# Performance work log

Measured on AMD Instinct MI355X. Metric: run time of the kernel, lower is better.

The kernel has to match this reference:

```python
import math
import jax, jax.numpy as jnp
import numpy as np

B, N, D = 4, 4096, 1024
H, DH = 16, 64  # D == H * DH


def setup_inputs() -> dict:
    key = jax.random.key(0)
    ks = jax.random.split(key, 7)
    s = 1.0 / math.sqrt(D)
    return {
        "tens": jax.random.normal(ks[0], (B, N, D), dtype=jnp.float32),
        "Wq": jax.random.normal(ks[1], (D, D), dtype=jnp.float32) * s,
        "bq": jax.random.normal(ks[2], (D,), dtype=jnp.float32) * 0.01,
        "Wk": jax.random.normal(ks[3], (D, D), dtype=jnp.float32) * s,
        "bk": jax.random.normal(ks[4], (D,), dtype=jnp.float32) * 0.01,
        "Wv": jax.random.normal(ks[5], (D, D), dtype=jnp.float32) * s,
        "bv": jax.random.normal(ks[6], (D,), dtype=jnp.float32) * 0.01,
    }


def reference(tens, Wq, bq, Wk, bk, Wv, bv):
    b, n, d = tens.shape
    # projections (torch Linear: x @ W^T + b)
    q = (tens @ Wq.T + bq).reshape(b, n, H, DH)  # [B,N,H,DH]
    k = (tens @ Wk.T + bk).reshape(b, n, H, DH)
    v = (tens @ Wv.T + bv).reshape(b, n, H, DH)
    scale = (1.0 / math.sqrt(DH)) / math.sqrt(n)
    # No softmax between QK^T and V => linear, reassociate as Q @ (K^T V)
    # to avoid the O(N^2) attention matrix; identical math.
    ktv = jnp.einsum("bnhd,bnhe->bhde", k, v)          # [B,H,DH,DH]
    out = jnp.einsum("bnhd,bhde->bnhe", q, ktv) * scale  # [B,N,H,DH]
    return out.reshape(b, n, d)
```

## Files before the change

kernel.cpp:

```cpp
#include <hip/hip_runtime.h>

typedef unsigned short ushort_t;
typedef __attribute__((ext_vector_type(8))) __bf16 bf16x8;
typedef __attribute__((ext_vector_type(8))) unsigned short ushort8;
typedef __attribute__((ext_vector_type(4))) unsigned short ushort4_t;
typedef __attribute__((ext_vector_type(4))) float floatx4;

__device__ inline unsigned short f2bf(float f) {
  union { float f; unsigned u; } x; x.f = f;
  return (unsigned short)((x.u + 0x7FFFu + ((x.u >> 16) & 1u)) >> 16);
}
__device__ inline float bf2f(unsigned short v) {
  union { unsigned u; float f; } x; x.u = (unsigned)v << 16;
  return x.f;
}

__device__ inline void bar() {
  asm volatile("" ::: "memory");
  __builtin_amdgcn_s_barrier();
  asm volatile("" ::: "memory");
}
#define WAITV0 asm volatile("s_waitcnt vmcnt(0)" ::: "memory")

__global__ void cvt_tr(const float* __restrict__ tens, ushort_t* __restrict__ Xbf,
                       ushort_t* __restrict__ XT, float* __restrict__ spart,
                       const float* __restrict__ Wk, ushort_t* __restrict__ Wkbf,
                       const float* __restrict__ Wv, ushort_t* __restrict__ Wvbf) {
  int t = threadIdx.x;
  if (blockIdx.z == 4) {
    int flat = blockIdx.x + 16 * blockIdx.y;
    const float* in; ushort_t* out;
    if (flat < 512) { in = Wk; out = Wkbf; } else { in = Wv; out = Wvbf; flat -= 512; }
    int i = (flat * 256 + t) * 8;
    const float4* p = (const float4*)(in + i);
    float4 x = p[0], y = p[1];
    ushort8 o;
    o[0] = f2bf(x.x); o[1] = f2bf(x.y); o[2] = f2bf(x.z); o[3] = f2bf(x.w);
    o[4] = f2bf(y.x); o[5] = f2bf(y.y); o[6] = f2bf(y.z); o[7] = f2bf(y.w);
    *(ushort8*)(out + i) = o;
    return;
  }
  int b = blockIdx.z;
  int d0 = blockIdx.x * 64;
  int n0 = blockIdx.y * 64;
  __shared__ ushort_t sT[64 * 72];
  int nl = t >> 2, c16 = (t & 3) * 16;
  const float* src = tens + ((long)b << 22) + (long)(n0 + nl) * 1024 + d0 + c16;
  ushort8 o0, o1;
#pragma unroll
  for (int j = 0; j < 2; ++j) {
    float4 v0 = *(const float4*)(src + j * 8);
    float4 v1 = *(const float4*)(src + j * 8 + 4);
    ushort8 o;
    o[0] = f2bf(v0.x); o[1] = f2bf(v0.y); o[2] = f2bf(v0.z); o[3] = f2bf(v0.w);
    o[4] = f2bf(v1.x); o[5] = f2bf(v1.y); o[6] = f2bf(v1.z); o[7] = f2bf(v1.w);
#pragma unroll
    for (int i = 0; i < 8; ++i) sT[(c16 + j * 8 + i) * 72 + nl] = o[i];
    if (j == 0) o0 = o; else o1 = o;
  }
  ushort_t* xdst = Xbf + ((long)b << 22) + (long)(n0 + nl) * 1024 + d0 + c16;
  *(ushort8*)xdst = o0;
  *(ushort8*)(xdst + 8) = o1;
  __syncthreads();
  int dl = t >> 2, n16 = (t & 3) * 16;
  ushort8 t0 = *(const ushort8*)(sT + dl * 72 + n16);
  ushort8 t1 = *(const ushort8*)(sT + dl * 72 + n16 + 8);
  ushort_t* dst = XT + ((long)b << 22) + (long)(d0 + dl) * 4096 + n0 + n16;
  *(ushort8*)dst = t0;
  *(ushort8*)(dst + 8) = t1;
  float ps = 0.f;
#pragma unroll
  for (int i = 0; i < 8; ++i) ps += bf2f(t0[i]) + bf2f(t1[i]);
  ps += __shfl_xor(ps, 1);
  ps += __shfl_xor(ps, 2);
  if ((t & 3) == 0) spart[(((long)b << 6) + blockIdx.y) * 1024 + d0 + dl] = ps;
}

__device__ inline void gload_lds16(const void* g, void* l) {
  __builtin_amdgcn_global_load_lds(
      (const __attribute__((address_space(1))) unsigned int*)g,
      (__attribute__((address_space(3))) unsigned int*)l, 16, 0, 0);
}

template <int K>
__global__ __launch_bounds__(512, 2) void gemm256(
    const ushort_t* __restrict__ A, const ushort_t* __restrict__ Bm,
    const float* __restrict__ bias, float* __restrict__ C,
    int N, long sA_, long sB_, long sBias_, long sC_) {
  const int NT = K / 64;
  int gx = gridDim.x, gxy = gridDim.x * gridDim.y;
  int flat = blockIdx.x + gx * blockIdx.y + gxy * blockIdx.z;
  int total = gxy * gridDim.z;
  int per = total >> 3;
  int nf = (flat & 7) * per + (flat >> 3);
  int bz = nf / gxy; int rem = nf - bz * gxy;
  int by = rem / gx; int bx = rem - by * gx;

  A += (long)bz * sA_; Bm += (long)bz * sB_; C += (long)bz * sC_;
  bias += (long)bz * sBias_;

  __shared__ ushort_t sA[2][16384];
  __shared__ ushort_t sB[2][16384];

  int t = threadIdx.x;
  int w = t >> 6, l = t & 63;
  int wy = w >> 2, wx = w & 3;
  int quad = l >> 4, m16 = l & 15;
  int mBase = by * 256, nBase = bx * 256;

  int rp = w * 8 + (l >> 3);
  int p8 = l & 7;
  int ce = ((p8 ^ (rp & 7)) << 3);
  const ushort_t* gAp[4]; const ushort_t* gBp[4];
#pragma unroll
  for (int h = 0; h < 2; ++h)
#pragma unroll
    for (int g = 0; g < 2; ++g) {
      gAp[h * 2 + g] = A + (long)(mBase + h * 128 + g * 64 + rp) * K + ce;
      gBp[h * 2 + g] = Bm + (long)(nBase + h * 128 + g * 64 + rp) * K + ce;
    }

  int swz3 = m16 & 7;
  int aBase = wy * 8192 + m16 * 64;
  int bBase = (wx >> 1) * 8192 + ((wx & 1) * 64 + m16) * 64;

  floatx4 acc[8][4] = {};

  auto STAGE = [&](int kt, int buf) {
    int ko = kt * 64;
#pragma unroll
    for (int g = 0; g < 2; ++g) {
      gload_lds16(gAp[g] + ko,     sA[buf] + g * 4096 + w * 512);
      gload_lds16(gAp[2 + g] + ko, sA[buf] + 8192 + g * 4096 + w * 512);
      gload_lds16(gBp[g] + ko,     sB[buf] + g * 4096 + w * 512);
      gload_lds16(gBp[2 + g] + ko, sB[buf] + 8192 + g * 4096 + w * 512);
    }
  };

  STAGE(0, 0);
  WAITV0;
  bar();
  for (int kt = 0; kt < NT; ++kt) {
    int buf = kt & 1;
    if (kt + 1 < NT) STAGE(kt + 1, buf ^ 1);
    __builtin_amdgcn_sched_barrier(0);
    const ushort_t* pa = sA[buf];
    const ushort_t* pb = sB[buf];
    __builtin_amdgcn_s_setprio(1);
#pragma unroll
    for (int ks = 0; ks < 2; ++ks) {
      int ct = (((ks * 4 + quad) ^ swz3) << 3);
      bf16x8 bfr[4];
#pragma unroll
      for (int ni = 0; ni < 4; ++ni)
        bfr[ni] = *(const bf16x8*)(pb + bBase + ni * 16 * 64 + ct);
#pragma unroll
      for (int mg = 0; mg < 2; ++mg) {
        bf16x8 af[4];
#pragma unroll
        for (int i = 0; i < 4; ++i)
          af[i] = *(const bf16x8*)(pa + aBase + (mg * 4 + i) * 16 * 64 + ct);
#pragma unroll
        for (int i = 0; i < 4; ++i)
#pragma unroll
          for (int ni = 0; ni < 4; ++ni)
            acc[mg * 4 + i][ni] = __builtin_amdgcn_mfma_f32_16x16x32_bf16(
                af[i], bfr[ni], acc[mg * 4 + i][ni], 0, 0, 0);
      }
    }
    __builtin_amdgcn_s_setprio(0);
    if (kt + 1 < NT) { WAITV0; }
    bar();
  }

#pragma unroll
  for (int ni = 0; ni < 4; ++ni) {
    int n = nBase + wx * 64 + ni * 16 + m16;
    float bb = bias[n];
#pragma unroll
    for (int mi = 0; mi < 8; ++mi) {
      int m0 = mBase + wy * 128 + mi * 16 + quad * 4;
      floatx4 v = acc[mi][ni];
#pragma unroll
      for (int rr = 0; rr < 4; ++rr)
        C[(long)(m0 + rr) * N + n] = v[rr] + bb;
    }
  }
}

template <int K, bool SYM, bool UW>
__global__ void gemm64(const ushort_t* __restrict__ A, const ushort_t* __restrict__ Bm,
                       ushort_t* __restrict__ C, int N, long sA_, long sB_, long sC_,
                       const ushort_t* __restrict__ Wkbf, const ushort_t* __restrict__ Wvbf,
                       const float* __restrict__ spart, float* __restrict__ u,
                       float* __restrict__ wv_s) {
  __shared__ ushort_t sA[2][2][64 * 32];
  __shared__ ushort_t sB[2][2][64 * 32];
  int t = threadIdx.x;

  int bz, byy, bxx;
  if (SYM) {
    int flat = blockIdx.x + gridDim.x * blockIdx.y;
    int per = (gridDim.x * gridDim.y) >> 3;
    int nf = (flat & 7) * per + (flat >> 3);
    if (UW) {
      if (nf >= 544) {
        int id = nf - 544;
        int b = id & 3, which = (id >> 2) & 1, chunk = id >> 3;
        const ushort_t* W = which ? Wvbf : Wkbf;
        float* o = which ? wv_s : u;
        float* ss = (float*)sA;
        float4 a4 = {0.f, 0.f, 0.f, 0.f};
        const float* sp = spart + ((long)b << 16) + t * 4;
        for (int n0 = 0; n0 < 64; ++n0) {
          float4 v = *(const float4*)(sp + n0 * 1024);
          a4.x += v.x; a4.y += v.y; a4.z += v.z; a4.w += v.w;
        }
        *(float4*)(ss + t * 4) = a4;
        __syncthreads();
        int rr = chunk * 256 + t;
        const ushort_t* row = W + (long)rr * 1024;
        float acc = 0.f;
        for (int k = 0; k < 1024; k += 8) {
          ushort8 v = *(const ushort8*)(row + k);
#pragma unroll
          for (int i = 0; i < 8; ++i) acc += bf2f(v[i]) * ss[k + i];
        }
        o[b * 1024 + rr] = acc;
        return;
      }
    }
    bz = nf / 136;
    int tri = nf - bz * 136;
    byy = (int)((__fsqrt_rn(8.0f * tri + 1.0f) - 1.0f) * 0.5f);
    while ((byy + 1) * (byy + 2) / 2 <= tri) ++byy;
    while (byy * (byy + 1) / 2 > tri) --byy;
    bxx = tri - byy * (byy + 1) / 2;
  } else {
    int gx = gridDim.x, gxy = gridDim.x * gridDim.y;
    int flat = blockIdx.x + gx * blockIdx.y + gxy * blockIdx.z;
    int total = gxy * gridDim.z;
    int per = total >> 3;
    int nf = (flat & 7) * per + (flat >> 3);
    bz = nf / gxy; int rem = nf - bz * gxy;
    byy = rem / gx; bxx = rem - byy * gx;
  }

  A += (long)bz * sA_; Bm += (long)bz * sB_; C += (long)bz * sC_;

  int w = t >> 6, l = t & 63;
  int wy = w >> 1, wx = w & 1;
  int quad = l >> 4, m16 = l & 15;
  int mBase = byy * 64, nBase = bxx * 64;

  int r = l >> 2, pk = l & 3;
  int sCol = (pk ^ ((r >> 1) & 3)) * 8;
  int sRow = w * 16 + r;
  const ushort_t* gA = A + (long)(mBase + sRow) * K + sCol;
  const ushort_t* gB = Bm + (long)(nBase + sRow) * K + sCol;
  int lOff = w * 512;

  int swzR = (m16 >> 1) & 3;
  int aOff = (wy * 32 + m16) * 32 + (quad ^ swzR) * 8;
  int bOff = (wx * 32 + m16) * 32 + (quad ^ swzR) * 8;

  floatx4 acc[2][2] = {};
  const int NS = K / 64;

#pragma unroll
  for (int kk = 0; kk < 2; ++kk) {
    gload_lds16(gA + kk * 32, sA[0][kk] + lOff);
    gload_lds16(gB + kk * 32, sB[0][kk] + lOff);
  }
  __syncthreads();

  for (int kt = 0; kt < NS; ++kt) {
    if (kt + 1 < NS) {
      int nb = (kt + 1) & 1, ko = (kt + 1) * 64;
#pragma unroll
      for (int kk = 0; kk < 2; ++kk) {
        gload_lds16(gA + ko + kk * 32, sA[nb][kk] + lOff);
        gload_lds16(gB + ko + kk * 32, sB[nb][kk] + lOff);
      }
    }
    __builtin_amdgcn_sched_barrier(0);
    int cb = kt & 1;
#pragma unroll
    for (int kk = 0; kk < 2; ++kk) {
      bf16x8 af0 = *(const bf16x8*)(sA[cb][kk] + aOff);
      bf16x8 af1 = *(const bf16x8*)(sA[cb][kk] + aOff + 16 * 32);
      bf16x8 bf0 = *(const bf16x8*)(sB[cb][kk] + bOff);
      bf16x8 bf1 = *(const bf16x8*)(sB[cb][kk] + bOff + 16 * 32);
      acc[0][0] = __builtin_amdgcn_mfma_f32_16x16x32_bf16(af0, bf0, acc[0][0], 0, 0, 0);
      acc[0][1] = __builtin_amdgcn_mfma_f32_16x16x32_bf16(af0, bf1, acc[0][1], 0, 0, 0);
      acc[1][0] = __builtin_amdgcn_mfma_f32_16x16x32_bf16(af1, bf0, acc[1][0], 0, 0, 0);
      acc[1][1] = __builtin_amdgcn_mfma_f32_16x16x32_bf16(af1, bf1, acc[1][1], 0, 0, 0);
    }
    if (kt + 1 < NS) __syncthreads();
  }

#pragma unroll
  for (int ni = 0; ni < 2; ++ni) {
    int n = nBase + wx * 32 + ni * 16 + m16;
#pragma unroll
    for (int mi = 0; mi < 2; ++mi) {
      int m0 = mBase + wy * 32 + mi * 16 + quad * 4;
      floatx4 v = acc[mi][ni];
#pragma unroll
      for (int rr = 0; rr < 4; ++rr)
        C[(long)(m0 + rr) * N + n] = f2bf(v[rr]);
      if (SYM) {
        if (byy != bxx) {
          ushort4_t pkv;
#pragma unroll
          for (int rr = 0; rr < 4; ++rr) pkv[rr] = f2bf(v[rr]);
          *(ushort4_t*)(C + (long)n * N + m0) = pkv;
        }
      }
    }
  }
}

__global__ void ktv_part_k(const ushort_t* __restrict__ T1, const ushort_t* __restrict__ Wvbf,
                           const float* __restrict__ u, const float* __restrict__ wv_s,
                           const float* __restrict__ bk, const float* __restrict__ bv,
                           float* __restrict__ ktvp) {
  int id = blockIdx.x;
  int bh = id & 63, sl = id >> 6;
  int b = bh >> 4, h = bh & 15;
  int t = threadIdx.x, w = t >> 6, l = t & 63;
  int quad = l >> 4, m16 = l & 15;
  const ushort_t* Arow = T1 + ((long)b << 20) + (long)(h * 64 + w * 16 + m16) * 1024
                         + sl * 256 + quad * 8;
  const ushort_t* Brow = Wvbf + (long)(h * 64 + m16) * 1024 + sl * 256 + quad * 8;
  floatx4 acc[4] = {};
  for (int kt = 0; kt < 256; kt += 32) {
    bf16x8 af = *(const bf16x8*)(Arow + kt);
#pragma unroll
    for (int j = 0; j < 4; ++j) {
      bf16x8 bfv = *(const bf16x8*)(Brow + (long)j * 16 * 1024 + kt);
      acc[j] = __builtin_amdgcn_mfma_f32_16x16x32_bf16(af, bfv, acc[j], 0, 0, 0);
    }
  }
  float* p = ktvp + ((long)(sl * 64 + bh)) * 4096;
#pragma unroll
  for (int j = 0; j < 4; ++j) {
    int e = j * 16 + m16;
    float bve = bv[h * 64 + e];
    float wse = wv_s[b * 1024 + h * 64 + e] + 4096.f * bve;
#pragma unroll
    for (int rr = 0; rr < 4; ++rr) {
      int d = w * 16 + quad * 4 + rr;
      float corr = (sl == 0)
          ? (u[b * 1024 + h * 64 + d] * bve + bk[h * 64 + d] * wse) : 0.f;
      p[d * 64 + e] = acc[j][rr] + corr;
    }
  }
}

__global__ void make_w2(const float* __restrict__ Wq, const float* __restrict__ bq,
                        const float* __restrict__ ktvp, ushort_t* __restrict__ W2T,
                        float* __restrict__ bias2, float scale) {
  int bh = blockIdx.x, cq = blockIdx.y;
  int b = bh >> 4, h = bh & 15;
  __shared__ float sKTV[64 * 64];
  __shared__ float sW[64 * 64];
  int t = threadIdx.x;
  const float* kp = ktvp + (long)bh * 4096;
  for (int i = t * 4; i < 4096; i += 1024) {
    float4 v0 = *(const float4*)(kp + i);
    float4 v1 = *(const float4*)(kp + 262144 + i);
    float4 v2 = *(const float4*)(kp + 524288 + i);
    float4 v3 = *(const float4*)(kp + 786432 + i);
    float4 s;
    s.x = v0.x + v1.x + v2.x + v3.x;
    s.y = v0.y + v1.y + v2.y + v3.y;
    s.z = v0.z + v1.z + v2.z + v3.z;
    s.w = v0.w + v1.w + v2.w + v3.w;
    *(float4*)(sKTV + i) = s;
  }
  __syncthreads();
  if (cq == 0 && t < 64) {
    float s = 0.f;
    for (int d = 0; d < 64; ++d) s += bq[h * 64 + d] * sKTV[d * 64 + t];
    bias2[b * 1024 + h * 64 + t] = s * scale;
  }
  int e = t >> 2, c0 = (t & 3) * 16;
  for (int ct = cq * 256; ct < cq * 256 + 256; ct += 64) {
    __syncthreads();
    {
      int d = t >> 2, cc = (t & 3) * 16;
#pragma unroll
      for (int j = 0; j < 16; j += 4)
        *(float4*)(sW + d * 64 + cc + j) =
            *(const float4*)(Wq + (long)(h * 64 + d) * 1024 + ct + cc + j);
    }
    __syncthreads();
    float outv[16] = {};
    for (int d = 0; d < 64; ++d) {
      float kv = sKTV[d * 64 + e];
#pragma unroll
      for (int j = 0; j < 16; ++j) outv[j] += sW[d * 64 + c0 + j] * kv;
    }
    ushort8 o0, o1;
#pragma unroll
    for (int j = 0; j < 8; ++j) { o0[j] = f2bf(outv[j] * scale); o1[j] = f2bf(outv[8 + j] * scale); }
    ushort_t* dst = W2T + ((long)(b * 1024 + h * 64 + e)) * 1024 + ct + c0;
    *(ushort8*)dst = o0;
    *(ushort8*)(dst + 8) = o1;
  }
}

extern "C" void kernel_launch(void* const* d_in, const int* in_sizes, int n_in,
                              void* d_out, int out_size, void* d_ws, size_t ws_size,
                              hipStream_t stream) {
  (void)in_sizes; (void)n_in; (void)out_size; (void)ws_size;
  const float* tens = (const float*)d_in[0];
  const float* Wq = (const float*)d_in[1];
  const float* bq = (const float*)d_in[2];
  const float* Wk = (const float*)d_in[3];
  const float* bk = (const float*)d_in[4];
  const float* Wv = (const float*)d_in[5];
  const float* bv = (const float*)d_in[6];
  float* out = (float*)d_out;

  char* w = (char*)d_ws;
  ushort_t* Xbf  = (ushort_t*)(w);
  ushort_t* XT   = (ushort_t*)(w + 33554432);
  ushort_t* Wkbf = (ushort_t*)(w + 67108864);
  ushort_t* Wvbf = (ushort_t*)(w + 69206016);
  ushort_t* Gbf  = (ushort_t*)(w + 71303168);
  ushort_t* T1   = (ushort_t*)(w + 79691776);
  float*    spart= (float*)(w + 88080384);
  float*    u    = (float*)(w + 89128960);
  float*    wv_s = (float*)(w + 89145344);
  float*    ktvp = (float*)(w + 89161728);
  ushort_t* W2T  = (ushort_t*)(w + 93356032);
  float*    bias2= (float*)(w + 101744640);

  const float scale = (1.0f / 8.0f) / 64.0f;

  hipLaunchKernelGGL(cvt_tr, dim3(16, 64, 5), dim3(256), 0, stream,
                     tens, Xbf, XT, spart, Wk, Wkbf, Wv, Wvbf);

  hipLaunchKernelGGL((gemm64<4096, true, true>), dim3(144, 4, 1), dim3(256), 0, stream,
                     XT, XT, Gbf, 1024, 4194304L, 4194304L, 1048576L,
                     Wkbf, Wvbf, spart, u, wv_s);

  hipLaunchKernelGGL((gemm64<1024, false, false>), dim3(16, 16, 4), dim3(256), 0, stream,
                     Wkbf, Gbf, T1, 1024, 0L, 1048576L, 1048576L,
                     (const ushort_t*)nullptr, (const ushort_t*)nullptr,
                     (const float*)nullptr, (float*)nullptr, (float*)nullptr);

  hipLaunchKernelGGL(ktv_part_k, dim3(256), dim3(256), 0, stream,
                     T1, Wvbf, u, wv_s, bk, bv, ktvp);

  hipLaunchKernelGGL(make_w2, dim3(64, 4), dim3(256), 0, stream,
                     Wq, bq, ktvp, W2T, bias2, scale);

  hipLaunchKernelGGL((gemm256<1024>), dim3(4, 16, 4), dim3(512), 0, stream,
                     Xbf, W2T, bias2, out, 1024,
                     4194304L, 1048576L, 1024L, 4194304L);
}
```

Before: 275.1 us.

## Fuse Wk·G projection into per-head KTV kernel and vectorize final GEMM stores

The separate T1 = Wk·G GEMM and the ktv_part kernel are merged into one kernel. Each block computes its 64x256 slice of T1 for one head and batch, keeps it in shared memory as bf16, and multiplies it against Wv directly. This removes the T1 round trip through global memory and one launch. In exchange, the fused kernel has only 256 blocks with a long K=1024 loop that reads directly from global memory without LDS tiling. Separately, the final GEMM swaps its MFMA operand order so each lane holds consecutive columns, which allows float4 bias loads and float4 output stores instead of strided scalar stores.

```diff
diff --git a/kernel.cpp b/kernel.cpp
--- a/kernel.cpp
+++ b/kernel.cpp
@@ -165,7 +165,7 @@
 #pragma unroll
           for (int ni = 0; ni < 4; ++ni)
             acc[mg * 4 + i][ni] = __builtin_amdgcn_mfma_f32_16x16x32_bf16(
-                af[i], bfr[ni], acc[mg * 4 + i][ni], 0, 0, 0);
+                bfr[ni], af[i], acc[mg * 4 + i][ni], 0, 0, 0);
       }
     }
     __builtin_amdgcn_s_setprio(0);
@@ -174,16 +174,17 @@
   }
 
 #pragma unroll
-  for (int ni = 0; ni < 4; ++ni) {
-    int n = nBase + wx * 64 + ni * 16 + m16;
-    float bb = bias[n];
-#pragma unroll
-    for (int mi = 0; mi < 8; ++mi) {
-      int m0 = mBase + wy * 128 + mi * 16 + quad * 4;
+  for (int mi = 0; mi < 8; ++mi) {
+    int m = mBase + wy * 128 + mi * 16 + m16;
+    float* crow = C + (long)m * N;
+#pragma unroll
+    for (int ni = 0; ni < 4; ++ni) {
+      int n0 = nBase + wx * 64 + ni * 16 + quad * 4;
+      float4 bb = *(const float4*)(bias + n0);
       floatx4 v = acc[mi][ni];
-#pragma unroll
-      for (int rr = 0; rr < 4; ++rr)
-        C[(long)(m0 + rr) * N + n] = v[rr] + bb;
+      float4 o;
+      o.x = v[0] + bb.x; o.y = v[1] + bb.y; o.z = v[2] + bb.z; o.w = v[3] + bb.w;
+      *(float4*)(crow + n0) = o;
     }
   }
 }
@@ -321,28 +322,46 @@
   }
 }
 
-__global__ void ktv_part_k(const ushort_t* __restrict__ T1, const ushort_t* __restrict__ Wvbf,
-                           const float* __restrict__ u, const float* __restrict__ wv_s,
-                           const float* __restrict__ bk, const float* __restrict__ bv,
-                           float* __restrict__ ktvp) {
-  int id = blockIdx.x;
-  int bh = id & 63, sl = id >> 6;
+__global__ void t1ktv(const ushort_t* __restrict__ Wkbf, const ushort_t* __restrict__ Gbf,
+                      const ushort_t* __restrict__ Wvbf,
+                      const float* __restrict__ u, const float* __restrict__ wv_s,
+                      const float* __restrict__ bk, const float* __restrict__ bv,
+                      float* __restrict__ ktvp) {
+  int bh = blockIdx.x, cq = blockIdx.y;
   int b = bh >> 4, h = bh & 15;
+  __shared__ ushort_t sT1[64 * 264];
   int t = threadIdx.x, w = t >> 6, l = t & 63;
   int quad = l >> 4, m16 = l & 15;
-  const ushort_t* Arow = T1 + ((long)b << 20) + (long)(h * 64 + w * 16 + m16) * 1024
-                         + sl * 256 + quad * 8;
-  const ushort_t* Brow = Wvbf + (long)(h * 64 + m16) * 1024 + sl * 256 + quad * 8;
-  floatx4 acc[4] = {};
+
+  const ushort_t* Arow = Wkbf + (long)(h * 64 + w * 16 + m16) * 1024 + quad * 8;
+  const ushort_t* Brow = Gbf + ((long)b << 20) + (long)(cq * 256 + m16) * 1024 + quad * 8;
+  floatx4 acc1[16] = {};
+  for (int kt = 0; kt < 1024; kt += 32) {
+    bf16x8 af = *(const bf16x8*)(Arow + kt);
+#pragma unroll
+    for (int j = 0; j < 16; ++j) {
+      bf16x8 bfv = *(const bf16x8*)(Brow + (long)j * 16 * 1024 + kt);
+      acc1[j] = __builtin_amdgcn_mfma_f32_16x16x32_bf16(af, bfv, acc1[j], 0, 0, 0);
+    }
+  }
+#pragma unroll
+  for (int j = 0; j < 16; ++j)
+#pragma unroll
+    for (int rr = 0; rr < 4; ++rr)
+      sT1[(w * 16 + quad * 4 + rr) * 264 + j * 16 + m16] = f2bf(acc1[j][rr]);
+  __syncthreads();
+
+  const ushort_t* Brow2 = Wvbf + (long)(h * 64 + m16) * 1024 + cq * 256 + quad * 8;
+  floatx4 acc2[4] = {};
   for (int kt = 0; kt < 256; kt += 32) {
-    bf16x8 af = *(const bf16x8*)(Arow + kt);
+    bf16x8 af2 = *(const bf16x8*)(sT1 + (w * 16 + m16) * 264 + quad * 8 + kt);
 #pragma unroll
     for (int j = 0; j < 4; ++j) {
-      bf16x8 bfv = *(const bf16x8*)(Brow + (long)j * 16 * 1024 + kt);
-      acc[j] = __builtin_amdgcn_mfma_f32_16x16x32_bf16(af, bfv, acc[j], 0, 0, 0);
-    }
-  }
-  float* p = ktvp + ((long)(sl * 64 + bh)) * 4096;
+      bf16x8 bfv = *(const bf16x8*)(Brow2 + (long)j * 16 * 1024 + kt);
+      acc2[j] = __builtin_amdgcn_mfma_f32_16x16x32_bf16(af2, bfv, acc2[j], 0, 0, 0);
+    }
+  }
+  float* p = ktvp + ((long)(cq * 64 + bh)) * 4096;
 #pragma unroll
   for (int j = 0; j < 4; ++j) {
     int e = j * 16 + m16;
@@ -351,9 +370,9 @@
 #pragma unroll
     for (int rr = 0; rr < 4; ++rr) {
       int d = w * 16 + quad * 4 + rr;
-      float corr = (sl == 0)
+      float corr = (cq == 0)
           ? (u[b * 1024 + h * 64 + d] * bve + bk[h * 64 + d] * wse) : 0.f;
-      p[d * 64 + e] = acc[j][rr] + corr;
+      p[d * 64 + e] = acc2[j][rr] + corr;
     }
   }
 }
@@ -430,13 +449,12 @@
   ushort_t* Wkbf = (ushort_t*)(w + 67108864);
   ushort_t* Wvbf = (ushort_t*)(w + 69206016);
   ushort_t* Gbf  = (ushort_t*)(w + 71303168);
-  ushort_t* T1   = (ushort_t*)(w + 79691776);
-  float*    spart= (float*)(w + 88080384);
-  float*    u    = (float*)(w + 89128960);
-  float*    wv_s = (float*)(w + 89145344);
-  float*    ktvp = (float*)(w + 89161728);
-  ushort_t* W2T  = (ushort_t*)(w + 93356032);
-  float*    bias2= (float*)(w + 101744640);
+  float*    spart= (float*)(w + 79691776);
+  float*    u    = (float*)(w + 80740352);
+  float*    wv_s = (float*)(w + 80756736);
+  float*    ktvp = (float*)(w + 80773120);
+  ushort_t* W2T  = (ushort_t*)(w + 84967424);
+  float*    bias2= (float*)(w + 93356032);
 
   const float scale = (1.0f / 8.0f) / 64.0f;
 
@@ -447,13 +465,8 @@
                      XT, XT, Gbf, 1024, 4194304L, 4194304L, 1048576L,
                      Wkbf, Wvbf, spart, u, wv_s);
 
-  hipLaunchKernelGGL((gemm64<1024, false, false>), dim3(16, 16, 4), dim3(256), 0, stream,
-                     Wkbf, Gbf, T1, 1024, 0L, 1048576L, 1048576L,
-                     (const ushort_t*)nullptr, (const ushort_t*)nullptr,
-                     (const float*)nullptr, (float*)nullptr, (float*)nullptr);
-
-  hipLaunchKernelGGL(ktv_part_k, dim3(256), dim3(256), 0, stream,
-                     T1, Wvbf, u, wv_s, bk, bv, ktvp);
+  hipLaunchKernelGGL(t1ktv, dim3(64, 4), dim3(256), 0, stream,
+                     Wkbf, Gbf, Wvbf, u, wv_s, bk, bv, ktvp);
 
   hipLaunchKernelGGL(make_w2, dim3(64, 4), dim3(256), 0, stream,
                      Wq, bq, ktvp, W2T, bias2, scale);
```

Result: slower. 360.5 us (+31.1%).
